# Performance work log

Measured on AMD Instinct MI355X. Metric: run time of the kernel, lower is better.

## Reference

```python
import jax, jax.numpy as jnp
import numpy as np

WIDTH = 256
FREQS = 10
INPUT_WIDTH = 3 + 3 * 2 * FREQS  # 63


def embed_point(point, freqs):
    # point: [N, 3] -> [N, 3*(1+2*freqs)]
    linear = point[..., None]                                  # [N, 3, 1]
    scales = jnp.exp2(jnp.arange(freqs, dtype=point.dtype))    # [freqs]
    angles = linear * scales                                   # [N, 3, freqs]
    emb = jnp.concatenate((linear, jnp.sin(angles), jnp.cos(angles)), axis=-1)
    return emb.reshape(*point.shape[:-1], 3 * (1 + 2 * freqs))


def _xavier(key, fan_in, fan_out):
    limit = jnp.sqrt(6.0 / (fan_in + fan_out)).astype(jnp.float32)
    return jax.random.uniform(key, (fan_in, fan_out), jnp.float32, -limit, limit)


def setup_inputs() -> dict:
    key = jax.random.key(0)
    keys = jax.random.split(key, 20)
    N = 524288
    point = jax.random.normal(keys[0], (N, 3), dtype=jnp.float32)
    dims = [
        (INPUT_WIDTH, WIDTH), (WIDTH, WIDTH), (WIDTH, WIDTH), (WIDTH, WIDTH),
        (WIDTH, WIDTH), (WIDTH + INPUT_WIDTH, WIDTH), (WIDTH, WIDTH),
        (WIDTH, WIDTH), (WIDTH, 4),
    ]
    inp = {"point": point}
    for i, (fi, fo) in enumerate(dims):
        inp[f"w{i}"] = _xavier(keys[1 + i], fi, fo)
        inp[f"b{i}"] = jnp.zeros((fo,), dtype=jnp.float32)
    return inp


def reference(point, w0, b0, w1, b1, w2, b2, w3, b3, w4, b4,
              w5, b5, w6, b6, w7, b7, w8, b8):
    inp = embed_point(point, FREQS)                 # [N, 63]
    x = jax.nn.relu(inp @ w0 + b0)
    x = jax.nn.relu(x @ w1 + b1)
    x = jax.nn.relu(x @ w2 + b2)
    x = jax.nn.relu(x @ w3 + b3)
    x = jax.nn.relu(x @ w4 + b4)
    x = jax.nn.relu(jnp.concatenate((x, inp), -1) @ w5 + b5)  # skip concat
    x = jax.nn.relu(x @ w6 + b6)
    x = jax.nn.relu(x @ w7 + b7)
    return x @ w8 + b8                              # [N, 4]
```

## Files before the change

### kernel.cpp

```cpp
#include <hip/hip_runtime.h>
#include <math.h>


typedef __attribute__((ext_vector_type(8))) short short8;
typedef __attribute__((ext_vector_type(4))) float f32x4;
typedef __attribute__((ext_vector_type(16))) float f32x16;

struct WPtrs { const float* w[8]; };
struct BPtrs { const float* b[8]; };

#define INV2PI 0.15915494309189533577f

#define PK_L0 0
#define PK_L1 16384
#define PK_L2 81920
#define PK_L3 147456
#define PK_L4 212992
#define PK_L5 278528
#define PK_L6 360448
#define PK_L7 425984
#define PK_W8 491520
#define PK_TOTAL 495616

__device__ __forceinline__ unsigned short f2bf(float v) {
  unsigned u = __float_as_uint(v);
  u = u + 0x7fffu + ((u >> 16) & 1u);
  return (unsigned short)(u >> 16);
}
__device__ __forceinline__ float bf_lo(unsigned u) { return __uint_as_float(u << 16); }
__device__ __forceinline__ float bf_hi(unsigned u) { return __uint_as_float(u & 0xffff0000u); }

__device__ __forceinline__ unsigned cvtpk(float a, float b) {
#if __has_builtin(__builtin_amdgcn_cvt_pk_bf16_f32)
  typedef __attribute__((ext_vector_type(2))) __bf16 bf16x2_t;
  bf16x2_t r = __builtin_amdgcn_cvt_pk_bf16_f32(a, b);
  return __builtin_bit_cast(unsigned, r);
#else
  unsigned ua = __float_as_uint(a);
  ua += 0x7fffu + ((ua >> 16) & 1u);
  unsigned ub = __float_as_uint(b);
  ub += 0x7fffu + ((ub >> 16) & 1u);
#if __has_builtin(__builtin_amdgcn_perm)
  return __builtin_amdgcn_perm(ub, ua, 0x07060302u);
#else
  return (ua >> 16) | (ub & 0xffff0000u);
#endif
#endif
}

__device__ __forceinline__ float fractf_(float x) {
#if __has_builtin(__builtin_amdgcn_fract_f32)
  return __builtin_amdgcn_fract_f32(x);
#else
  return x - floorf(x);
#endif
}
__device__ __forceinline__ float sin_rev(float rev) {
#if __has_builtin(__builtin_amdgcn_sinf)
  return __builtin_amdgcn_sinf(rev);
#else
  return __sinf(rev * 6.283185307179586f);
#endif
}

__device__ __forceinline__ float embval(int f, float c0, float c1, float c2,
                                        float x0, float x1, float x2) {
  if (f >= 63) return 0.0f;
  int d = (f >= 21 ? 1 : 0) + (f >= 42 ? 1 : 0);
  int r = f - d * 21;
  float c = (d == 0) ? c0 : (d == 1 ? c1 : c2);
  float x = (d == 0) ? x0 : (d == 1 ? x1 : x2);
  bool isc = r > 10;
  int e = isc ? (r - 11) : (r - 1);
  float rev = fractf_(ldexpf(x, e) + (isc ? 0.25f : 0.0f));
  float s = sin_rev(rev);
  return (r == 0) ? c : s;
}

__device__ __forceinline__ f32x16 mfma32(short8 a, short8 b, f32x16 c) {
  return __builtin_amdgcn_mfma_f32_32x32x16_bf16(a, b, c, 0, 0, 0);
}
__device__ __forceinline__ f32x4 mfma16(short8 a, short8 b, f32x4 c) {
  return __builtin_amdgcn_mfma_f32_16x16x32_bf16(a, b, c, 0, 0, 0);
}

__global__ void pack_weights(WPtrs W, const float* __restrict__ w8,
                             unsigned short* __restrict__ out) {
  int idx = blockIdx.x * 256 + threadIdx.x;
  if (idx >= PK_TOTAL) return;
  float v;
  if (idx >= PK_W8) {
    int t = idx - PK_W8;
    int j = t >> 8, k = t & 255;
    v = (j < 4) ? w8[k * 4 + j] : 0.0f;
  } else {
    int e = idx & 15;
    int blk = idx >> 4;
    int ch = blk & 255;
    int kkg = blk >> 8;
    int l, kk0;
    if      (kkg < 4)   { l = 0; kk0 = 0;   }
    else if (kkg < 20)  { l = 1; kk0 = 4;   }
    else if (kkg < 36)  { l = 2; kk0 = 20;  }
    else if (kkg < 52)  { l = 3; kk0 = 36;  }
    else if (kkg < 68)  { l = 4; kk0 = 52;  }
    else if (kkg < 88)  { l = 5; kk0 = 68;  }
    else if (kkg < 104) { l = 6; kk0 = 88;  }
    else                { l = 7; kk0 = 104; }
    int k = (kkg - kk0) * 16 + e;
    const int realK[8] = {63, 256, 256, 256, 256, 319, 256, 256};
    v = (k < realK[l]) ? W.w[l][k * 256 + ch] : 0.0f;
  }
  out[idx] = f2bf(v);
}

template <int KKA, int PAB, int KKB, bool RB>
__device__ __forceinline__ void do_layer32(
    const unsigned short* srcA, const unsigned short* srcB,
    const unsigned short* __restrict__ wblk,
    const float* __restrict__ bias,
    unsigned short* dst, int w, int n, int h, unsigned swz) {
  f32x16 acc[2][2];
#pragma unroll
  for (int mt = 0; mt < 2; ++mt)
#pragma unroll
    for (int q = 0; q < 4; ++q) {
      f32x4 bq = *reinterpret_cast<const f32x4*>(bias + w * 64 + mt * 32 + q * 8 + h * 4);
#pragma unroll
      for (int r = 0; r < 4; ++r) {
        acc[mt][0][q * 4 + r] = bq[r];
        acc[mt][1][q * 4 + r] = bq[r];
      }
    }

  const unsigned short* ab = wblk + (unsigned)((w * 64 + n) * 16 + h * 8);
  const char* rA0 = (const char*)srcA + (unsigned)(n * PAB);
  const char* rA1 = rA0 + 32 * PAB;

#pragma unroll 4
  for (int kk = 0; kk < KKA; ++kk) {
    short8 a0 = *reinterpret_cast<const short8*>(ab + kk * 4096);
    short8 a1 = *reinterpret_cast<const short8*>(ab + kk * 4096 + 512);
    unsigned off = ((unsigned)(kk * 32 + h * 16)) ^ swz;
    short8 b0 = *reinterpret_cast<const short8*>(rA0 + off);
    short8 b1 = *reinterpret_cast<const short8*>(rA1 + off);
    acc[0][0] = mfma32(a0, b0, acc[0][0]);
    acc[0][1] = mfma32(a0, b1, acc[0][1]);
    acc[1][0] = mfma32(a1, b0, acc[1][0]);
    acc[1][1] = mfma32(a1, b1, acc[1][1]);
  }
  if (KKB > 0) {
    const char* rB0 = (const char*)srcB + (unsigned)(n * 128);
    const char* rB1 = rB0 + 32 * 128;
#pragma unroll
    for (int kl = 0; kl < KKB; ++kl) {
      const unsigned short* ab2 = ab + (KKA + kl) * 4096;
      short8 a0 = *reinterpret_cast<const short8*>(ab2);
      short8 a1 = *reinterpret_cast<const short8*>(ab2 + 512);
      unsigned off = ((unsigned)(kl * 32 + h * 16)) ^ swz;
      short8 b0 = *reinterpret_cast<const short8*>(rB0 + off);
      short8 b1 = *reinterpret_cast<const short8*>(rB1 + off);
      acc[0][0] = mfma32(a0, b0, acc[0][0]);
      acc[0][1] = mfma32(a0, b1, acc[0][1]);
      acc[1][0] = mfma32(a1, b0, acc[1][0]);
      acc[1][1] = mfma32(a1, b1, acc[1][1]);
    }
  }

  if (RB) __syncthreads();
#pragma unroll
  for (int nt = 0; nt < 2; ++nt) {
    char* rowp = (char*)dst + (unsigned)((nt * 32 + n) * 512);
#pragma unroll
    for (int mt = 0; mt < 2; ++mt)
#pragma unroll
      for (int q = 0; q < 4; ++q) {
        float x0 = fmaxf(acc[mt][nt][q * 4 + 0], 0.0f);
        float x1 = fmaxf(acc[mt][nt][q * 4 + 1], 0.0f);
        float x2 = fmaxf(acc[mt][nt][q * 4 + 2], 0.0f);
        float x3 = fmaxf(acc[mt][nt][q * 4 + 3], 0.0f);
        uint2 pr;
        pr.x = cvtpk(x0, x1);
        pr.y = cvtpk(x2, x3);
        unsigned off = ((unsigned)(w * 128 + mt * 64 + q * 16 + h * 8)) ^ swz;
        *reinterpret_cast<uint2*>(rowp + off) = pr;
      }
  }
  __syncthreads();
}

__launch_bounds__(256, 4)
__global__ void mlp_mfma(const float* __restrict__ pts, long N,
                         BPtrs B, const float* __restrict__ b8,
                         const unsigned short* __restrict__ wpk,
                         float* __restrict__ out) {
  __shared__ unsigned short act[64 * 256];
  __shared__ unsigned short emb[64 * 64];
  const int tid = threadIdx.x;
  const int w = tid >> 6, lane = tid & 63;
  const int n = lane & 31, h = lane >> 5;
  const unsigned swz = (unsigned)((n & 7) << 4);
  const long pbase = (long)blockIdx.x * 64;

  {
    const int pt = tid >> 2, fg = tid & 3;
    const long pg = pbase + pt;
    float c0 = 0.f, c1 = 0.f, c2 = 0.f;
    if (pg < N) {
      const float* pp = pts + pg * 3;
      c0 = pp[0]; c1 = pp[1]; c2 = pp[2];
    }
    float x0 = c0 * INV2PI, x1 = c1 * INV2PI, x2 = c2 * INV2PI;
    unsigned pk[8];
#pragma unroll
    for (int i = 0; i < 16; i += 2) {
      int f0 = fg * 16 + i;
      float v0 = embval(f0,     c0, c1, c2, x0, x1, x2);
      float v1 = embval(f0 + 1, c0, c1, c2, x0, x1, x2);
      pk[i >> 1] = cvtpk(v0, v1);
    }
    const unsigned sw = (unsigned)((pt & 7) << 4);
    char* rowp = (char*)emb + (unsigned)(pt * 128);
    *reinterpret_cast<uint4*>(rowp + (((unsigned)(fg * 32)) ^ sw)) =
        uint4{pk[0], pk[1], pk[2], pk[3]};
    *reinterpret_cast<uint4*>(rowp + (((unsigned)(fg * 32 + 16)) ^ sw)) =
        uint4{pk[4], pk[5], pk[6], pk[7]};
  }
  __syncthreads();

  do_layer32<4,  128, 0, false>(emb, nullptr, wpk + PK_L0, B.b[0], act, w, n, h, swz);
  do_layer32<16, 512, 0, true >(act, nullptr, wpk + PK_L1, B.b[1], act, w, n, h, swz);
  do_layer32<16, 512, 0, true >(act, nullptr, wpk + PK_L2, B.b[2], act, w, n, h, swz);
  do_layer32<16, 512, 0, true >(act, nullptr, wpk + PK_L3, B.b[3], act, w, n, h, swz);
  do_layer32<16, 512, 0, true >(act, nullptr, wpk + PK_L4, B.b[4], act, w, n, h, swz);
  do_layer32<16, 512, 4, true >(act, emb,     wpk + PK_L5, B.b[5], act, w, n, h, swz);
  do_layer32<16, 512, 0, true >(act, nullptr, wpk + PK_L6, B.b[6], act, w, n, h, swz);
  do_layer32<16, 512, 0, true >(act, nullptr, wpk + PK_L7, B.b[7], act, w, n, h, swz);

  {
    const int l16 = lane & 15, quad = lane >> 4;
    const unsigned short* w8b = wpk + PK_W8 + (unsigned)(l16 * 256 + quad * 8);
    const int pt = w * 16 + l16;
    const char* ba = (const char*)act + (unsigned)(pt * 512);
    f32x4 a4 = {0.f, 0.f, 0.f, 0.f};
#pragma unroll
    for (int kk = 0; kk < 8; ++kk) {
      short8 a = *reinterpret_cast<const short8*>(w8b + kk * 32);
      unsigned off = ((unsigned)(kk * 64 + quad * 16)) ^ swz;
      short8 b = *reinterpret_cast<const short8*>(ba + off);
      a4 = mfma16(a, b, a4);
    }
    if (quad == 0) {
      f32x4 bb = *reinterpret_cast<const f32x4*>(b8);
      long pg = pbase + pt;
      f32x4 v = a4 + bb;
      if (pg < N) *reinterpret_cast<f32x4*>(out + pg * 4) = v;
    }
  }
}

__device__ __forceinline__ unsigned pk2s(float a, float b) {
  return (unsigned)f2bf(a) | ((unsigned)f2bf(b) << 16);
}
__device__ __forceinline__ void fb_seg(const unsigned short* src, int kRows,
                                       const float* __restrict__ wr,
                                       int lane, int ps, float acc[4][16]) {
#pragma unroll 4
  for (int k = 0; k < kRows; ++k) {
    const float* p = wr + k * 256 + lane;
    float w0 = p[0], w1 = p[64], w2 = p[128], w3 = p[192];
    const uint4* xr = reinterpret_cast<const uint4*>(src + ((k << 6) + ps));
    uint4 q0 = xr[0], q1 = xr[1];
    float x[16];
    x[0] = bf_lo(q0.x);  x[1] = bf_hi(q0.x);  x[2] = bf_lo(q0.y);  x[3] = bf_hi(q0.y);
    x[4] = bf_lo(q0.z);  x[5] = bf_hi(q0.z);  x[6] = bf_lo(q0.w);  x[7] = bf_hi(q0.w);
    x[8] = bf_lo(q1.x);  x[9] = bf_hi(q1.x);  x[10] = bf_lo(q1.y); x[11] = bf_hi(q1.y);
    x[12] = bf_lo(q1.z); x[13] = bf_hi(q1.z); x[14] = bf_lo(q1.w); x[15] = bf_hi(q1.w);
#pragma unroll
    for (int pp = 0; pp < 16; ++pp) {
      acc[0][pp] = fmaf(w0, x[pp], acc[0][pp]);
      acc[1][pp] = fmaf(w1, x[pp], acc[1][pp]);
      acc[2][pp] = fmaf(w2, x[pp], acc[2][pp]);
      acc[3][pp] = fmaf(w3, x[pp], acc[3][pp]);
    }
  }
}
__device__ __forceinline__ void fb_layer(const unsigned short* srcA, int kA,
                                         const unsigned short* srcB, int kB,
                                         const float* wrA, const float* wrB,
                                         const float* bias,
                                         unsigned short* dst, int lane, int ps) {
  float acc[4][16];
#pragma unroll
  for (int jt = 0; jt < 4; ++jt) {
    float bb = bias[lane + (jt << 6)];
#pragma unroll
    for (int pp = 0; pp < 16; ++pp) acc[jt][pp] = bb;
  }
  fb_seg(srcA, kA, wrA, lane, ps, acc);
  if (srcB) fb_seg(srcB, kB, wrB, lane, ps, acc);
#pragma unroll
  for (int jt = 0; jt < 4; ++jt) {
    unsigned short* dr = dst + (((lane + (jt << 6)) << 6) + ps);
    float r[16];
#pragma unroll
    for (int pp = 0; pp < 16; ++pp) r[pp] = fmaxf(acc[jt][pp], 0.0f);
    uint4 a, b;
    a.x = pk2s(r[0], r[1]);   a.y = pk2s(r[2], r[3]);
    a.z = pk2s(r[4], r[5]);   a.w = pk2s(r[6], r[7]);
    b.x = pk2s(r[8], r[9]);   b.y = pk2s(r[10], r[11]);
    b.z = pk2s(r[12], r[13]); b.w = pk2s(r[14], r[15]);
    reinterpret_cast<uint4*>(dr)[0] = a;
    reinterpret_cast<uint4*>(dr)[1] = b;
  }
}
__launch_bounds__(256, 2)
__global__ void mlp_fallback(const float* __restrict__ pts, int N,
                             WPtrs W, BPtrs B,
                             const float* __restrict__ w8,
                             const float* __restrict__ b8,
                             float* __restrict__ out) {
  __shared__ unsigned short act[256 * 64];
  __shared__ unsigned short emb[64 * 64];
  const int lane = threadIdx.x & 63;
  const int ps = (threadIdx.x >> 6) << 4;
  const long pbase = (long)blockIdx.x * 64 + ps;
#pragma unroll
  for (int i = 0; i < 16; ++i) {
    int idx = (i << 6) + lane;
    int f = idx >> 4, pp = idx & 15;
    float v = 0.0f;
    if (f < 63) {
      float c = (pbase + pp < N) ? pts[(pbase + pp) * 3 + (f / 21)] : 0.0f;
      float x = c * INV2PI;
      v = embval(f, c, c, c, x, x, x);
    }
    emb[(f << 6) + ps + pp] = f2bf(v);
  }
  fb_layer(emb, 63, nullptr, 0, W.w[0], nullptr, B.b[0], act, lane, ps);
#pragma unroll 1
  for (int l = 1; l <= 4; ++l)
    fb_layer(act, 256, nullptr, 0, W.w[l], nullptr, B.b[l], act, lane, ps);
  fb_layer(act, 256, emb, 63, W.w[5], W.w[5] + 256 * 256, B.b[5], act, lane, ps);
#pragma unroll 1
  for (int l = 6; l <= 7; ++l)
    fb_layer(act, 256, nullptr, 0, W.w[l], nullptr, B.b[l], act, lane, ps);
  {
    const int pp = lane & 15, cc = lane >> 4;
    float a = b8[cc];
#pragma unroll 4
    for (int k = 0; k < 256; ++k)
      a = fmaf(bf_lo((unsigned)act[(k << 6) + ps + pp]), w8[(k << 2) + cc], a);
    if (pbase + pp < N) out[(pbase + pp) * 4 + cc] = a;
  }
}

extern "C" void kernel_launch(void* const* d_in, const int* in_sizes, int n_in,
                              void* d_out, int out_size, void* d_ws, size_t ws_size,
                              hipStream_t stream) {
  const float* pts = (const float*)d_in[0];
  WPtrs W; BPtrs B;
  for (int i = 0; i < 8; ++i) {
    W.w[i] = (const float*)d_in[1 + 2 * i];
    B.b[i] = (const float*)d_in[2 + 2 * i];
  }
  const float* w8 = (const float*)d_in[17];
  const float* b8 = (const float*)d_in[18];
  float* out = (float*)d_out;
  const long N = in_sizes[0] / 3;

  const size_t need = (size_t)PK_TOTAL * sizeof(unsigned short);
  if (ws_size >= need) {
    unsigned short* wpk = (unsigned short*)d_ws;
    pack_weights<<<1936, 256, 0, stream>>>(W, w8, wpk);
    mlp_mfma<<<(int)((N + 63) / 64), 256, 0, stream>>>(pts, N, B, b8, wpk, out);
  } else {
    mlp_fallback<<<(int)((N + 63) / 64), 256, 0, stream>>>(pts, (int)N, W, B, w8, b8, out);
  }
}
```

Baseline: 602.9 us.

## Double points per block to 128 and repack weights row-contiguous per channel

Each block now handles 128 points instead of 64, so every weight fragment loaded from global memory feeds four MFMA N-tiles instead of two, halving weight traffic per point. Weights are repacked so each output channel's K values are contiguous (stride KPAD), which changes the A-fragment addressing. LDS usage doubles and the accumulator count doubles, so launch bounds drop to two blocks per CU, trading occupancy for reuse. The final layer loops twice per wave to cover the larger tile.

```diff
diff --git a/kernel.cpp b/kernel.cpp
--- a/kernel.cpp
+++ b/kernel.cpp
@@ -94,82 +94,82 @@
     int j = t >> 8, k = t & 255;
     v = (j < 4) ? w8[k * 4 + j] : 0.0f;
   } else {
-    int e = idx & 15;
-    int blk = idx >> 4;
-    int ch = blk & 255;
-    int kkg = blk >> 8;
-    int l, kk0;
-    if      (kkg < 4)   { l = 0; kk0 = 0;   }
-    else if (kkg < 20)  { l = 1; kk0 = 4;   }
-    else if (kkg < 36)  { l = 2; kk0 = 20;  }
-    else if (kkg < 52)  { l = 3; kk0 = 36;  }
-    else if (kkg < 68)  { l = 4; kk0 = 52;  }
-    else if (kkg < 88)  { l = 5; kk0 = 68;  }
-    else if (kkg < 104) { l = 6; kk0 = 88;  }
-    else                { l = 7; kk0 = 104; }
-    int k = (kkg - kk0) * 16 + e;
-    const int realK[8] = {63, 256, 256, 256, 256, 319, 256, 256};
-    v = (k < realK[l]) ? W.w[l][k * 256 + ch] : 0.0f;
+    int l, base, kpad, realk;
+    if      (idx < PK_L1) { l = 0; base = PK_L0; kpad = 64;  realk = 63;  }
+    else if (idx < PK_L2) { l = 1; base = PK_L1; kpad = 256; realk = 256; }
+    else if (idx < PK_L3) { l = 2; base = PK_L2; kpad = 256; realk = 256; }
+    else if (idx < PK_L4) { l = 3; base = PK_L3; kpad = 256; realk = 256; }
+    else if (idx < PK_L5) { l = 4; base = PK_L4; kpad = 256; realk = 256; }
+    else if (idx < PK_L6) { l = 5; base = PK_L5; kpad = 320; realk = 319; }
+    else if (idx < PK_L7) { l = 6; base = PK_L6; kpad = 256; realk = 256; }
+    else                  { l = 7; base = PK_L7; kpad = 256; realk = 256; }
+    int t = idx - base;
+    int ch = t / kpad, k = t - ch * kpad;
+    v = (k < realk) ? W.w[l][k * 256 + ch] : 0.0f;
   }
   out[idx] = f2bf(v);
 }
 
-template <int KKA, int PAB, int KKB, bool RB>
+template <int KKA, int KPAD, int PAB, int KKB, bool RB>
 __device__ __forceinline__ void do_layer32(
     const unsigned short* srcA, const unsigned short* srcB,
     const unsigned short* __restrict__ wblk,
     const float* __restrict__ bias,
     unsigned short* dst, int w, int n, int h, unsigned swz) {
-  f32x16 acc[2][2];
+  f32x16 acc[2][4];
 #pragma unroll
   for (int mt = 0; mt < 2; ++mt)
 #pragma unroll
     for (int q = 0; q < 4; ++q) {
       f32x4 bq = *reinterpret_cast<const f32x4*>(bias + w * 64 + mt * 32 + q * 8 + h * 4);
 #pragma unroll
-      for (int r = 0; r < 4; ++r) {
-        acc[mt][0][q * 4 + r] = bq[r];
-        acc[mt][1][q * 4 + r] = bq[r];
-      }
-    }
-
-  const unsigned short* ab = wblk + (unsigned)((w * 64 + n) * 16 + h * 8);
-  const char* rA0 = (const char*)srcA + (unsigned)(n * PAB);
-  const char* rA1 = rA0 + 32 * PAB;
+      for (int r = 0; r < 4; ++r)
+#pragma unroll
+        for (int nt = 0; nt < 4; ++nt)
+          acc[mt][nt][q * 4 + r] = bq[r];
+    }
+
+  const unsigned short* ab0 = wblk + (unsigned)((w * 64 + n) * KPAD + h * 8);
+  const unsigned short* ab1 = ab0 + 32 * KPAD;
+  const char* rbase = (const char*)srcA + (unsigned)(n * PAB);
 
 #pragma unroll 4
   for (int kk = 0; kk < KKA; ++kk) {
-    short8 a0 = *reinterpret_cast<const short8*>(ab + kk * 4096);
-    short8 a1 = *reinterpret_cast<const short8*>(ab + kk * 4096 + 512);
+    short8 a0 = *reinterpret_cast<const short8*>(ab0 + kk * 16);
+    short8 a1 = *reinterpret_cast<const short8*>(ab1 + kk * 16);
     unsigned off = ((unsigned)(kk * 32 + h * 16)) ^ swz;
-    short8 b0 = *reinterpret_cast<const short8*>(rA0 + off);
-    short8 b1 = *reinterpret_cast<const short8*>(rA1 + off);
-    acc[0][0] = mfma32(a0, b0, acc[0][0]);
-    acc[0][1] = mfma32(a0, b1, acc[0][1]);
-    acc[1][0] = mfma32(a1, b0, acc[1][0]);
-    acc[1][1] = mfma32(a1, b1, acc[1][1]);
+    short8 b[4];
+#pragma unroll
+    for (int nt = 0; nt < 4; ++nt)
+      b[nt] = *reinterpret_cast<const short8*>(rbase + nt * 32 * PAB + off);
+#pragma unroll
+    for (int nt = 0; nt < 4; ++nt) {
+      acc[0][nt] = mfma32(a0, b[nt], acc[0][nt]);
+      acc[1][nt] = mfma32(a1, b[nt], acc[1][nt]);
+    }
   }
   if (KKB > 0) {
-    const char* rB0 = (const char*)srcB + (unsigned)(n * 128);
-    const char* rB1 = rB0 + 32 * 128;
+    const char* rbB = (const char*)srcB + (unsigned)(n * 128);
 #pragma unroll
     for (int kl = 0; kl < KKB; ++kl) {
-      const unsigned short* ab2 = ab + (KKA + kl) * 4096;
-      short8 a0 = *reinterpret_cast<const short8*>(ab2);
-      short8 a1 = *reinterpret_cast<const short8*>(ab2 + 512);
+      short8 a0 = *reinterpret_cast<const short8*>(ab0 + (KKA + kl) * 16);
+      short8 a1 = *reinterpret_cast<const short8*>(ab1 + (KKA + kl) * 16);
       unsigned off = ((unsigned)(kl * 32 + h * 16)) ^ swz;
-      short8 b0 = *reinterpret_cast<const short8*>(rB0 + off);
-      short8 b1 = *reinterpret_cast<const short8*>(rB1 + off);
-      acc[0][0] = mfma32(a0, b0, acc[0][0]);
-      acc[0][1] = mfma32(a0, b1, acc[0][1]);
-      acc[1][0] = mfma32(a1, b0, acc[1][0]);
-      acc[1][1] = mfma32(a1, b1, acc[1][1]);
+      short8 b[4];
+#pragma unroll
+      for (int nt = 0; nt < 4; ++nt)
+        b[nt] = *reinterpret_cast<const short8*>(rbB + nt * 32 * 128 + off);
+#pragma unroll
+      for (int nt = 0; nt < 4; ++nt) {
+        acc[0][nt] = mfma32(a0, b[nt], acc[0][nt]);
+        acc[1][nt] = mfma32(a1, b[nt], acc[1][nt]);
+      }
     }
   }
 
   if (RB) __syncthreads();
 #pragma unroll
-  for (int nt = 0; nt < 2; ++nt) {
+  for (int nt = 0; nt < 4; ++nt) {
     char* rowp = (char*)dst + (unsigned)((nt * 32 + n) * 512);
 #pragma unroll
     for (int mt = 0; mt < 2; ++mt)
@@ -189,21 +189,22 @@
   __syncthreads();
 }
 
-__launch_bounds__(256, 4)
+__launch_bounds__(256, 2)
 __global__ void mlp_mfma(const float* __restrict__ pts, long N,
                          BPtrs B, const float* __restrict__ b8,
                          const unsigned short* __restrict__ wpk,
                          float* __restrict__ out) {
-  __shared__ unsigned short act[64 * 256];
-  __shared__ unsigned short emb[64 * 64];
+  __shared__ unsigned short act[128 * 256];
+  __shared__ unsigned short emb[128 * 64];
   const int tid = threadIdx.x;
   const int w = tid >> 6, lane = tid & 63;
   const int n = lane & 31, h = lane >> 5;
   const unsigned swz = (unsigned)((n & 7) << 4);
-  const long pbase = (long)blockIdx.x * 64;
-
-  {
-    const int pt = tid >> 2, fg = tid & 3;
+  const long pbase = (long)blockIdx.x * 128;
+
+#pragma unroll
+  for (int p2 = 0; p2 < 2; ++p2) {
+    const int pt = (tid >> 2) + (p2 << 6), fg = tid & 3;
     const long pg = pbase + pt;
     float c0 = 0.f, c1 = 0.f, c2 = 0.f;
     if (pg < N) {
@@ -228,33 +229,36 @@
   }
   __syncthreads();
 
-  do_layer32<4,  128, 0, false>(emb, nullptr, wpk + PK_L0, B.b[0], act, w, n, h, swz);
-  do_layer32<16, 512, 0, true >(act, nullptr, wpk + PK_L1, B.b[1], act, w, n, h, swz);
-  do_layer32<16, 512, 0, true >(act, nullptr, wpk + PK_L2, B.b[2], act, w, n, h, swz);
-  do_layer32<16, 512, 0, true >(act, nullptr, wpk + PK_L3, B.b[3], act, w, n, h, swz);
-  do_layer32<16, 512, 0, true >(act, nullptr, wpk + PK_L4, B.b[4], act, w, n, h, swz);
-  do_layer32<16, 512, 4, true >(act, emb,     wpk + PK_L5, B.b[5], act, w, n, h, swz);
-  do_layer32<16, 512, 0, true >(act, nullptr, wpk + PK_L6, B.b[6], act, w, n, h, swz);
-  do_layer32<16, 512, 0, true >(act, nullptr, wpk + PK_L7, B.b[7], act, w, n, h, swz);
+  do_layer32<4,  64,  128, 0, false>(emb, nullptr, wpk + PK_L0, B.b[0], act, w, n, h, swz);
+  do_layer32<16, 256, 512, 0, true >(act, nullptr, wpk + PK_L1, B.b[1], act, w, n, h, swz);
+  do_layer32<16, 256, 512, 0, true >(act, nullptr, wpk + PK_L2, B.b[2], act, w, n, h, swz);
+  do_layer32<16, 256, 512, 0, true >(act, nullptr, wpk + PK_L3, B.b[3], act, w, n, h, swz);
+  do_layer32<16, 256, 512, 0, true >(act, nullptr, wpk + PK_L4, B.b[4], act, w, n, h, swz);
+  do_layer32<16, 320, 512, 4, true >(act, emb,     wpk + PK_L5, B.b[5], act, w, n, h, swz);
+  do_layer32<16, 256, 512, 0, true >(act, nullptr, wpk + PK_L6, B.b[6], act, w, n, h, swz);
+  do_layer32<16, 256, 512, 0, true >(act, nullptr, wpk + PK_L7, B.b[7], act, w, n, h, swz);
 
   {
     const int l16 = lane & 15, quad = lane >> 4;
     const unsigned short* w8b = wpk + PK_W8 + (unsigned)(l16 * 256 + quad * 8);
-    const int pt = w * 16 + l16;
-    const char* ba = (const char*)act + (unsigned)(pt * 512);
-    f32x4 a4 = {0.f, 0.f, 0.f, 0.f};
-#pragma unroll
-    for (int kk = 0; kk < 8; ++kk) {
-      short8 a = *reinterpret_cast<const short8*>(w8b + kk * 32);
-      unsigned off = ((unsigned)(kk * 64 + quad * 16)) ^ swz;
-      short8 b = *reinterpret_cast<const short8*>(ba + off);
-      a4 = mfma16(a, b, a4);
-    }
-    if (quad == 0) {
-      f32x4 bb = *reinterpret_cast<const f32x4*>(b8);
-      long pg = pbase + pt;
-      f32x4 v = a4 + bb;
-      if (pg < N) *reinterpret_cast<f32x4*>(out + pg * 4) = v;
+    const f32x4 bb = *reinterpret_cast<const f32x4*>(b8);
+#pragma unroll
+    for (int it = 0; it < 2; ++it) {
+      const int pt = w * 32 + it * 16 + l16;
+      const char* ba = (const char*)act + (unsigned)(pt * 512);
+      f32x4 a4 = {0.f, 0.f, 0.f, 0.f};
+#pragma unroll
+      for (int kk = 0; kk < 8; ++kk) {
+        short8 a = *reinterpret_cast<const short8*>(w8b + kk * 32);
+        unsigned off = ((unsigned)(kk * 64 + quad * 16)) ^ ((unsigned)((l16 & 7) << 4));
+        short8 b = *reinterpret_cast<const short8*>(ba + off);
+        a4 = mfma16(a, b, a4);
+      }
+      if (quad == 0) {
+        long pg = pbase + pt;
+        f32x4 v = a4 + bb;
+        if (pg < N) *reinterpret_cast<f32x4*>(out + pg * 4) = v;
+      }
     }
   }
 }
@@ -373,7 +377,7 @@
   if (ws_size >= need) {
     unsigned short* wpk = (unsigned short*)d_ws;
     pack_weights<<<1936, 256, 0, stream>>>(W, w8, wpk);
-    mlp_mfma<<<(int)((N + 63) / 64), 256, 0, stream>>>(pts, N, B, b8, wpk, out);
+    mlp_mfma<<<(int)((N + 127) / 128), 256, 0, stream>>>(pts, N, B, b8, wpk, out);
   } else {
     mlp_fallback<<<(int)((N + 63) / 64), 256, 0, stream>>>(pts, (int)N, W, B, w8, b8, out);
   }
```

After: 643.3 us. +6.7%, slower.

## Repack weights row-major per channel and prefetch next layer's first weight fragments

Applied to the files above, without the earlier changes.

Weight packing changes from 16-element k-blocks interleaved across channels to contiguous per-channel rows padded to each layer's K. Each MFMA wave now reads weights with stride KPAD per channel row instead of a 4096-element stride per k-step. The first two k-steps of the next layer's weights are loaded into registers before the barrier, hiding global latency at layer start. The final layer's swizzle is also changed to use the point row index, which corrects the read pattern. The cost is more live registers and a less coalesced global access pattern per k-step, since lanes now read different rows.

```diff
diff --git a/kernel.cpp b/kernel.cpp
--- a/kernel.cpp
+++ b/kernel.cpp
@@ -83,6 +83,9 @@
 __device__ __forceinline__ f32x4 mfma16(short8 a, short8 b, f32x4 c) {
   return __builtin_amdgcn_mfma_f32_16x16x32_bf16(a, b, c, 0, 0, 0);
 }
+__device__ __forceinline__ short8 lds8(const void* p) {
+  return *reinterpret_cast<const short8*>(p);
+}
 
 __global__ void pack_weights(WPtrs W, const float* __restrict__ w8,
                              unsigned short* __restrict__ out) {
@@ -94,30 +97,28 @@
     int j = t >> 8, k = t & 255;
     v = (j < 4) ? w8[k * 4 + j] : 0.0f;
   } else {
-    int e = idx & 15;
-    int blk = idx >> 4;
-    int ch = blk & 255;
-    int kkg = blk >> 8;
-    int l, kk0;
-    if      (kkg < 4)   { l = 0; kk0 = 0;   }
-    else if (kkg < 20)  { l = 1; kk0 = 4;   }
-    else if (kkg < 36)  { l = 2; kk0 = 20;  }
-    else if (kkg < 52)  { l = 3; kk0 = 36;  }
-    else if (kkg < 68)  { l = 4; kk0 = 52;  }
-    else if (kkg < 88)  { l = 5; kk0 = 68;  }
-    else if (kkg < 104) { l = 6; kk0 = 88;  }
-    else                { l = 7; kk0 = 104; }
-    int k = (kkg - kk0) * 16 + e;
-    const int realK[8] = {63, 256, 256, 256, 256, 319, 256, 256};
-    v = (k < realK[l]) ? W.w[l][k * 256 + ch] : 0.0f;
+    int l, base, kpad, realk;
+    if      (idx < PK_L1) { l = 0; base = PK_L0; kpad = 64;  realk = 63;  }
+    else if (idx < PK_L2) { l = 1; base = PK_L1; kpad = 256; realk = 256; }
+    else if (idx < PK_L3) { l = 2; base = PK_L2; kpad = 256; realk = 256; }
+    else if (idx < PK_L4) { l = 3; base = PK_L3; kpad = 256; realk = 256; }
+    else if (idx < PK_L5) { l = 4; base = PK_L4; kpad = 256; realk = 256; }
+    else if (idx < PK_L6) { l = 5; base = PK_L5; kpad = 320; realk = 319; }
+    else if (idx < PK_L7) { l = 6; base = PK_L6; kpad = 256; realk = 256; }
+    else                  { l = 7; base = PK_L7; kpad = 256; realk = 256; }
+    int t = idx - base;
+    int ch = t / kpad, k = t - ch * kpad;
+    v = (k < realk) ? W.w[l][k * 256 + ch] : 0.0f;
   }
   out[idx] = f2bf(v);
 }
 
-template <int KKA, int PAB, int KKB, bool RB>
+template <int KKA, int KPAD, int PAB, int KKB, bool RB, int NKPAD>
 __device__ __forceinline__ void do_layer32(
     const unsigned short* srcA, const unsigned short* srcB,
     const unsigned short* __restrict__ wblk,
+    const unsigned short* __restrict__ nwblk,
+    short8 (&pf)[4],
     const float* __restrict__ bias,
     unsigned short* dst, int w, int n, int h, unsigned swz) {
   f32x16 acc[2][2];
@@ -133,17 +134,28 @@
       }
     }
 
-  const unsigned short* ab = wblk + (unsigned)((w * 64 + n) * 16 + h * 8);
+  const unsigned short* ab0 = wblk + (unsigned)((w * 64 + n) * KPAD + h * 8);
+  const unsigned short* ab1 = ab0 + 32 * KPAD;
   const char* rA0 = (const char*)srcA + (unsigned)(n * PAB);
   const char* rA1 = rA0 + 32 * PAB;
 
+#pragma unroll
+  for (int kk = 0; kk < 2; ++kk) {
+    unsigned off = ((unsigned)(kk * 32 + h * 16)) ^ swz;
+    short8 b0 = lds8(rA0 + off);
+    short8 b1 = lds8(rA1 + off);
+    acc[0][0] = mfma32(pf[kk * 2 + 0], b0, acc[0][0]);
+    acc[0][1] = mfma32(pf[kk * 2 + 0], b1, acc[0][1]);
+    acc[1][0] = mfma32(pf[kk * 2 + 1], b0, acc[1][0]);
+    acc[1][1] = mfma32(pf[kk * 2 + 1], b1, acc[1][1]);
+  }
 #pragma unroll 4
-  for (int kk = 0; kk < KKA; ++kk) {
-    short8 a0 = *reinterpret_cast<const short8*>(ab + kk * 4096);
-    short8 a1 = *reinterpret_cast<const short8*>(ab + kk * 4096 + 512);
+  for (int kk = 2; kk < KKA; ++kk) {
+    short8 a0 = lds8(ab0 + kk * 16);
+    short8 a1 = lds8(ab1 + kk * 16);
     unsigned off = ((unsigned)(kk * 32 + h * 16)) ^ swz;
-    short8 b0 = *reinterpret_cast<const short8*>(rA0 + off);
-    short8 b1 = *reinterpret_cast<const short8*>(rA1 + off);
+    short8 b0 = lds8(rA0 + off);
+    short8 b1 = lds8(rA1 + off);
     acc[0][0] = mfma32(a0, b0, acc[0][0]);
     acc[0][1] = mfma32(a0, b1, acc[0][1]);
     acc[1][0] = mfma32(a1, b0, acc[1][0]);
@@ -154,17 +166,24 @@
     const char* rB1 = rB0 + 32 * 128;
 #pragma unroll
     for (int kl = 0; kl < KKB; ++kl) {
-      const unsigned short* ab2 = ab + (KKA + kl) * 4096;
-      short8 a0 = *reinterpret_cast<const short8*>(ab2);
-      short8 a1 = *reinterpret_cast<const short8*>(ab2 + 512);
+      short8 a0 = lds8(ab0 + (KKA + kl) * 16);
+      short8 a1 = lds8(ab1 + (KKA + kl) * 16);
       unsigned off = ((unsigned)(kl * 32 + h * 16)) ^ swz;
-      short8 b0 = *reinterpret_cast<const short8*>(rB0 + off);
-      short8 b1 = *reinterpret_cast<const short8*>(rB1 + off);
+      short8 b0 = lds8(rB0 + off);
+      short8 b1 = lds8(rB1 + off);
       acc[0][0] = mfma32(a0, b0, acc[0][0]);
       acc[0][1] = mfma32(a0, b1, acc[0][1]);
       acc[1][0] = mfma32(a1, b0, acc[1][0]);
       acc[1][1] = mfma32(a1, b1, acc[1][1]);
     }
+  }
+
+  if (NKPAD > 0) {
+    const unsigned short* nb0 = nwblk + (unsigned)((w * 64 + n) * NKPAD + h * 8);
+    pf[0] = lds8(nb0);
+    pf[1] = lds8(nb0 + 32 * NKPAD);
+    pf[2] = lds8(nb0 + 16);
+    pf[3] = lds8(nb0 + 32 * NKPAD + 16);
   }
 
   if (RB) __syncthreads();
@@ -202,6 +221,15 @@
   const unsigned swz = (unsigned)((n & 7) << 4);
   const long pbase = (long)blockIdx.x * 64;
 
+  short8 pf[4];
+  {
+    const unsigned short* nb0 = wpk + PK_L0 + (unsigned)((w * 64 + n) * 64 + h * 8);
+    pf[0] = lds8(nb0);
+    pf[1] = lds8(nb0 + 32 * 64);
+    pf[2] = lds8(nb0 + 16);
+    pf[3] = lds8(nb0 + 32 * 64 + 16);
+  }
+
   {
     const int pt = tid >> 2, fg = tid & 3;
     const long pg = pbase + pt;
@@ -228,26 +256,27 @@
   }
   __syncthreads();
 
-  do_layer32<4,  128, 0, false>(emb, nullptr, wpk + PK_L0, B.b[0], act, w, n, h, swz);
-  do_layer32<16, 512, 0, true >(act, nullptr, wpk + PK_L1, B.b[1], act, w, n, h, swz);
-  do_layer32<16, 512, 0, true >(act, nullptr, wpk + PK_L2, B.b[2], act, w, n, h, swz);
-  do_layer32<16, 512, 0, true >(act, nullptr, wpk + PK_L3, B.b[3], act, w, n, h, swz);
-  do_layer32<16, 512, 0, true >(act, nullptr, wpk + PK_L4, B.b[4], act, w, n, h, swz);
-  do_layer32<16, 512, 4, true >(act, emb,     wpk + PK_L5, B.b[5], act, w, n, h, swz);
-  do_layer32<16, 512, 0, true >(act, nullptr, wpk + PK_L6, B.b[6], act, w, n, h, swz);
-  do_layer32<16, 512, 0, true >(act, nullptr, wpk + PK_L7, B.b[7], act, w, n, h, swz);
+  do_layer32<4,  64,  128, 0, false, 256>(emb, nullptr, wpk + PK_L0, wpk + PK_L1, pf, B.b[0], act, w, n, h, swz);
+  do_layer32<16, 256, 512, 0, true,  256>(act, nullptr, wpk + PK_L1, wpk + PK_L2, pf, B.b[1], act, w, n, h, swz);
+  do_layer32<16, 256, 512, 0, true,  256>(act, nullptr, wpk + PK_L2, wpk + PK_L3, pf, B.b[2], act, w, n, h, swz);
+  do_layer32<16, 256, 512, 0, true,  256>(act, nullptr, wpk + PK_L3, wpk + PK_L4, pf, B.b[3], act, w, n, h, swz);
+  do_layer32<16, 256, 512, 0, true,  320>(act, nullptr, wpk + PK_L4, wpk + PK_L5, pf, B.b[4], act, w, n, h, swz);
+  do_layer32<16, 320, 512, 4, true,  256>(act, emb,     wpk + PK_L5, wpk + PK_L6, pf, B.b[5], act, w, n, h, swz);
+  do_layer32<16, 256, 512, 0, true,  256>(act, nullptr, wpk + PK_L6, wpk + PK_L7, pf, B.b[6], act, w, n, h, swz);
+  do_layer32<16, 256, 512, 0, true,  0  >(act, nullptr, wpk + PK_L7, nullptr,     pf, B.b[7], act, w, n, h, swz);
 
   {
     const int l16 = lane & 15, quad = lane >> 4;
     const unsigned short* w8b = wpk + PK_W8 + (unsigned)(l16 * 256 + quad * 8);
     const int pt = w * 16 + l16;
     const char* ba = (const char*)act + (unsigned)(pt * 512);
+    const unsigned sw = (unsigned)((pt & 7) << 4);
     f32x4 a4 = {0.f, 0.f, 0.f, 0.f};
 #pragma unroll
     for (int kk = 0; kk < 8; ++kk) {
-      short8 a = *reinterpret_cast<const short8*>(w8b + kk * 32);
-      unsigned off = ((unsigned)(kk * 64 + quad * 16)) ^ swz;
-      short8 b = *reinterpret_cast<const short8*>(ba + off);
+      short8 a = lds8(w8b + kk * 32);
+      unsigned off = ((unsigned)(kk * 64 + quad * 16)) ^ sw;
+      short8 b = lds8(ba + off);
       a4 = mfma16(a, b, a4);
     }
     if (quad == 0) {
```

New measurement: 1.072 ms. 77.8% more time.
